# Kernel optimization log

Hardware: AMD Instinct MI355X
Metric: run time of the kernel (lower is better)

Reference implementation:

```python
import jax, jax.numpy as jnp
from jax import lax
import numpy as np

H = 16        # hidden_size == input_size
L = 8         # num_layers


def _lstm_layer(x_seq, Wih, Whh, bih, bhh):
    # x_seq: [B, T, H] -> outputs [B, T, H]; PyTorch gate order i,f,g,o
    B = x_seq.shape[0]
    b = bih + bhh  # [4H]

    def step(carry, xt):
        h, c = carry
        gates = xt @ Wih.T + h @ Whh.T + b  # [B, 4H]
        i, f, g, o = jnp.split(gates, 4, axis=-1)
        c = jax.nn.sigmoid(f) * c + jax.nn.sigmoid(i) * jnp.tanh(g)
        h = jax.nn.sigmoid(o) * jnp.tanh(c)
        return (h, c), h

    h0 = jnp.zeros((B, H), x_seq.dtype)
    (_, _), hs = lax.scan(step, (h0, h0), jnp.swapaxes(x_seq, 0, 1))
    return jnp.swapaxes(hs, 0, 1)  # [B, T, H]


def setup_inputs() -> dict:
    key = jax.random.key(0)
    ks = jax.random.split(key, 9)
    s = 1.0 / np.sqrt(H)  # PyTorch default init scale
    x = jax.random.normal(ks[0], (2048, 512, H), dtype=jnp.float32)
    W_ih = jax.random.uniform(ks[1], (L, 4 * H, H), jnp.float32, -s, s)
    W_hh = jax.random.uniform(ks[2], (L, 4 * H, H), jnp.float32, -s, s)
    b_ih = jax.random.uniform(ks[3], (L, 4 * H), jnp.float32, -s, s)
    b_hh = jax.random.uniform(ks[4], (L, 4 * H), jnp.float32, -s, s)
    Wp = jax.random.uniform(ks[5], (3, H), jnp.float32, -s, s)
    bp = jax.random.uniform(ks[6], (3,), jnp.float32, -s, s)
    Wo = jax.random.uniform(ks[7], (3, H), jnp.float32, -s, s)
    bo = jax.random.uniform(ks[8], (3,), jnp.float32, -s, s)
    return {"x": x, "W_ih": W_ih, "W_hh": W_hh, "b_ih": b_ih, "b_hh": b_hh,
            "Wp": Wp, "bp": bp, "Wo": Wo, "bo": bo}


def reference(x, W_ih, W_hh, b_ih, b_hh, Wp, bp, Wo, bo):
    h = x
    for l in range(L):  # fixed small layer count
        h = _lstm_layer(h, W_ih[l], W_hh[l], b_ih[l], b_hh[l])
    last = h[:, -1, :]                       # [B, H]
    position = last @ Wp.T + bp              # [B, 3]
    orientation = jnp.tanh(last @ Wo.T + bo) # [B, 3]
    return jnp.concatenate((position, orientation), axis=1)  # [B, 6]
```

## Files before the change

### kernel.cpp

```cpp
#include <hip/hip_runtime.h>
#include <math.h>

typedef _Float16 f16x8 __attribute__((ext_vector_type(8)));
typedef float    f32x4 __attribute__((ext_vector_type(4)));

constexpr int kT     = 512;
constexpr int kH     = 16;
constexpr int kL     = 8;
constexpr int kNB    = 4;
constexpr int kSlots = 8;
constexpr int kLyr   = kL + 1;
constexpr int kRows  = 5;
constexpr int kRowE  = 16;
constexpr int kSE    = kLyr * kRows * kRowE;
constexpr int kEpochs= 136;

constexpr float kL2E = 1.4426950408889634f;

__device__ __forceinline__ float ex2(float w)  { return __builtin_amdgcn_exp2f(w); }
__device__ __forceinline__ float rcpf(float e) { return __builtin_amdgcn_rcpf(e); }

__global__ __launch_bounds__(512, 4)
void lstm_e4(const float* __restrict__ x,
             const float* __restrict__ Wih, const float* __restrict__ Whh,
             const float* __restrict__ bih, const float* __restrict__ bhh,
             const float* __restrict__ Wp,  const float* __restrict__ bpos,
             const float* __restrict__ Wo,  const float* __restrict__ bori,
             float* __restrict__ out)
{
    const int tid  = threadIdx.x;
    const int l    = tid >> 6;
    const int lane = tid & 63;
    const int n    = lane & 15;
    const int q    = lane >> 4;
    const int bl   = n & 3;
    const int g2   = (n >> 2) & 1;
    const int hi   = n >> 3;
    const bool bact = ((q >> 1) == g2);

    __shared__ __align__(16) _Float16 hb[kSlots][kLyr][kRows][kRowE];

    {
        int* hz = (int*)&hb[0][0][0][0];
        for (int i = tid; i < (int)(sizeof(hb) / 4); i += 512) hz[i] = 0;
    }
    __syncthreads();

    const float asc = ((n & 3) == 2) ? (-2.0f * kL2E) : (-kL2E);
    auto loadA = [&](const float* W, int T) -> f16x8 {
        const int wrow = (n & 3) * 16 + (n >> 2) + 4 * (q >> 1) + 8 * T;
        const float* src = W + (size_t)l * 64 * kH + wrow * kH;
        f16x8 a;
        #pragma unroll
        for (int j = 0; j < 8; ++j)
            a[j] = (_Float16)(asc * src[(q & 1) * 8 + j]);
        return a;
    };
    const f16x8 A1T0 = loadA(Wih, 0), A1T1 = loadA(Wih, 1);
    const f16x8 A2T0 = loadA(Whh, 0), A2T1 = loadA(Whh, 1);

    const int u0b = q + 4 * g2;
    f32x4 biasT0, biasT1;
    #pragma unroll
    for (int r = 0; r < 4; ++r) {
        const float sc = (r == 2) ? (-2.0f * kL2E) : (-kL2E);
        const int g0 = l * 64 + r * 16 + u0b;
        biasT0[r] = sc * (bih[g0] + bhh[g0]);
        biasT1[r] = sc * (bih[g0 + 8] + bhh[g0 + 8]);
    }

    const int boff = (bact ? bl * kRowE : 4 * kRowE) + (q & 1) * 8;
    const _Float16* b1b = &hb[0][l    ][0][0] + boff;
    const _Float16* b2b = &hb[0][l + 1][0][0] + boff;
    const int um = u0b + 8 * hi;
    _Float16* hw = &hb[0][l + 1][bl][um];
    _Float16* xw = &hb[0][0][bl][um];

    const float* xg = x + ((size_t)(blockIdx.x * kNB + bl) * kT) * kH + um;
    float xr[4] = {0.f, 0.f, 0.f, 0.f};
    if (l == 0) {
        #pragma unroll
        for (int t = 0; t < 8; ++t)
            hb[t][0][bl][um] = (_Float16)xg[(size_t)t * kH];
        #pragma unroll
        for (int j = 0; j < 4; ++j)
            xr[j] = xg[(size_t)(8 + j) * kH];
    }

    f16x8 B2r;
    #pragma unroll
    for (int j = 0; j < 8; ++j) B2r[j] = (_Float16)0.f;
    float c0 = 0.f;
    int te   = -4 * l;
    int sOfs = (l & 1) ? 4 * kSE : 0;

    #pragma unroll 1
    for (int ep = 0; ep < kEpochs; ++ep) {
        const _Float16* b1p = b1b + sOfs;
        const _Float16* b2p = b2b + sOfs;
        _Float16* hwp = hw + sOfs;
        _Float16* xwp = xw + sOfs;

        #pragma unroll
        for (int j = 0; j < 4; ++j) {
            const int t = te + j;
            const bool active = ((unsigned)t < (unsigned)kT);

            const f16x8 B1 = *(const f16x8*)(b1p + j * kSE);

            f32x4 dInT0 = __builtin_amdgcn_mfma_f32_16x16x32_f16(A1T0, B1, biasT0, 0, 0, 0);
            f32x4 dInT1 = __builtin_amdgcn_mfma_f32_16x16x32_f16(A1T1, B1, biasT1, 0, 0, 0);
            f32x4 dT0   = __builtin_amdgcn_mfma_f32_16x16x32_f16(A2T0, B2r, dInT0, 0, 0, 0);
            f32x4 dT1   = __builtin_amdgcn_mfma_f32_16x16x32_f16(A2T1, B2r, dInT1, 0, 0, 0);

            f32x4 d;
            #pragma unroll
            for (int r = 0; r < 4; ++r) d[r] = hi ? dT1[r] : dT0[r];

            const float Ei = ex2(fminf(d[0], 40.0f));
            const float Ef = ex2(fminf(d[1], 40.0f));
            const float Eg = ex2(fminf(d[2], 40.0f));
            const float Eo = ex2(fminf(d[3], 60.0f));
            const float Dg = 1.0f + Eg;
            const float Df = 1.0f + Ef;
            const float P1  = fmaf(Ei, Dg, Dg);
            const float den = Df * P1;
            const float t2  = fmaf(-Eg, Df, Df);
            const float num = fmaf(c0, P1, t2);
            float cn = num * rcpf(den);
            cn = active ? cn : 0.0f;
            c0 = cn;
            const float ac = fminf(cn * (-2.0f * kL2E), 60.0f);
            const float Ec = ex2(ac);
            const float Do = 1.0f + Eo;
            const float R2 = rcpf(fmaf(Do, Ec, Do));
            const float h0 = fmaf(-Ec, R2, R2);

            *(hwp + j * kSE) = (_Float16)h0;
            B2r = *(const f16x8*)(b2p + j * kSE);

            if (l == 0) {
                *(xwp + j * kSE) = (_Float16)xr[j];
                int ti = te + 12 + j; if (ti > kT - 1) ti = kT - 1;
                xr[j] = xg[(size_t)ti * kH];
            }
        }

        te += 4;
        sOfs ^= 4 * kSE;
        asm volatile("s_waitcnt lgkmcnt(0)\n\ts_barrier" ::: "memory");
    }

    __syncthreads();

    if (l == kL - 1 && lane < 32) {
        const int bb = lane >> 3;
        const int r  = lane & 7;
        if (r < 6) {
            const bool  isP   = (r < 3);
            const float* wrow = isP ? (Wp + r * kH) : (Wo + (r - 3) * kH);
            float acc = isP ? bpos[r] : bori[r - 3];
            #pragma unroll
            for (int u = 0; u < kH; ++u)
                acc = fmaf((float)hb[7][kL][bb][u], wrow[u], acc);
            if (!isP) {
                const float Et = ex2(-2.0f * kL2E * acc);
                acc = fmaf(2.0f, rcpf(1.0f + Et), -1.0f);
            }
            out[(size_t)(blockIdx.x * kNB + bb) * 6 + r] = acc;
        }
    }
}

extern "C" void kernel_launch(void* const* d_in, const int* in_sizes, int n_in,
                              void* d_out, int out_size, void* d_ws, size_t ws_size,
                              hipStream_t stream) {
    const float* x    = (const float*)d_in[0];
    const float* Wih  = (const float*)d_in[1];
    const float* Whh  = (const float*)d_in[2];
    const float* bih  = (const float*)d_in[3];
    const float* bhh  = (const float*)d_in[4];
    const float* Wp   = (const float*)d_in[5];
    const float* bpos = (const float*)d_in[6];
    const float* Wo   = (const float*)d_in[7];
    const float* bori = (const float*)d_in[8];
    float* out = (float*)d_out;

    const int B = in_sizes[0] / (kT * kH);
    lstm_e4<<<dim3(B / kNB), dim3(512), 0, stream>>>(x, Wih, Whh, bih, bhh,
                                                     Wp, bpos, Wo, bori, out);
}
```

Measured before the change: 303.5 us.

## Pass recurrent hidden state via ds_bpermute and shrink layer wavefront to 2-step epochs

Each wave now builds its own recurrent h operand in registers, using a lane shuffle plus ds_bpermute, instead of reading it back from shared memory. The epoch drops from 4 timesteps to 2 and the layer skew halves from 4 to 2 steps per layer, so the pipeline fill and drain are shorter, at the cost of twice as many barriers. The barrier waits with lgkmcnt(4) so the outstanding bpermutes can overlap it. The aim is to take the LDS store-then-reload latency off the serial dependency chain between timesteps.

```diff
diff --git a/kernel.cpp b/kernel.cpp
--- a/kernel.cpp
+++ b/kernel.cpp
@@ -13,7 +13,7 @@
 constexpr int kRows  = 5;
 constexpr int kRowE  = 16;
 constexpr int kSE    = kLyr * kRows * kRowE;
-constexpr int kEpochs= 136;
+constexpr int kEp    = 263;
 
 constexpr float kL2E = 1.4426950408889634f;
 
@@ -21,12 +21,12 @@
 __device__ __forceinline__ float rcpf(float e) { return __builtin_amdgcn_rcpf(e); }
 
 __global__ __launch_bounds__(512, 4)
-void lstm_e4(const float* __restrict__ x,
-             const float* __restrict__ Wih, const float* __restrict__ Whh,
-             const float* __restrict__ bih, const float* __restrict__ bhh,
-             const float* __restrict__ Wp,  const float* __restrict__ bpos,
-             const float* __restrict__ Wo,  const float* __restrict__ bori,
-             float* __restrict__ out)
+void lstm_bp2(const float* __restrict__ x,
+              const float* __restrict__ Wih, const float* __restrict__ Whh,
+              const float* __restrict__ bih, const float* __restrict__ bhh,
+              const float* __restrict__ Wp,  const float* __restrict__ bpos,
+              const float* __restrict__ Wo,  const float* __restrict__ bori,
+              float* __restrict__ out)
 {
     const int tid  = threadIdx.x;
     const int l    = tid >> 6;
@@ -70,53 +70,62 @@
     }
 
     const int boff = (bact ? bl * kRowE : 4 * kRowE) + (q & 1) * 8;
-    const _Float16* b1b = &hb[0][l    ][0][0] + boff;
-    const _Float16* b2b = &hb[0][l + 1][0][0] + boff;
+    const _Float16* b1b = &hb[0][l][0][0] + boff;
     const int um = u0b + 8 * hi;
     _Float16* hw = &hb[0][l + 1][bl][um];
     _Float16* xw = &hb[0][0][bl][um];
 
+    int bpa[4];
+    #pragma unroll
+    for (int d = 0; d < 4; ++d) {
+        const int v0 = (q & 1) * 8 + 2 * d;
+        const int Lh = 16 * (v0 & 3) + bl + 4 * ((v0 >> 2) & 1) + 8 * (v0 >> 3);
+        bpa[d] = 4 * Lh;
+    }
+    const int msk = bact ? ~0 : 0;
+
     const float* xg = x + ((size_t)(blockIdx.x * kNB + bl) * kT) * kH + um;
-    float xr[4] = {0.f, 0.f, 0.f, 0.f};
+    float xr0 = 0.f, xr1 = 0.f, xr2 = 0.f, xr3 = 0.f;
     if (l == 0) {
         #pragma unroll
         for (int t = 0; t < 8; ++t)
             hb[t][0][bl][um] = (_Float16)xg[(size_t)t * kH];
-        #pragma unroll
-        for (int j = 0; j < 4; ++j)
-            xr[j] = xg[(size_t)(8 + j) * kH];
-    }
-
-    f16x8 B2r;
-    #pragma unroll
-    for (int j = 0; j < 8; ++j) B2r[j] = (_Float16)0.f;
+        xr0 = xg[ 8 * (size_t)kH];
+        xr1 = xg[ 9 * (size_t)kH];
+        xr2 = xg[10 * (size_t)kH];
+        xr3 = xg[11 * (size_t)kH];
+    }
+    __syncthreads();
+
+    int nb0 = 0, nb1 = 0, nb2 = 0, nb3 = 0;
     float c0 = 0.f;
-    int te   = -4 * l;
-    int sOfs = (l & 1) ? 4 * kSE : 0;
+    int te   = -2 * l;
+    int offA = ((-2 * l) & 7) * kSE;
 
     #pragma unroll 1
-    for (int ep = 0; ep < kEpochs; ++ep) {
-        const _Float16* b1p = b1b + sOfs;
-        const _Float16* b2p = b2b + sOfs;
-        _Float16* hwp = hw + sOfs;
-        _Float16* xwp = xw + sOfs;
-
-        #pragma unroll
-        for (int j = 0; j < 4; ++j) {
-            const int t = te + j;
-            const bool active = ((unsigned)t < (unsigned)kT);
-
-            const f16x8 B1 = *(const f16x8*)(b1p + j * kSE);
-
-            f32x4 dInT0 = __builtin_amdgcn_mfma_f32_16x16x32_f16(A1T0, B1, biasT0, 0, 0, 0);
-            f32x4 dInT1 = __builtin_amdgcn_mfma_f32_16x16x32_f16(A1T1, B1, biasT1, 0, 0, 0);
-            f32x4 dT0   = __builtin_amdgcn_mfma_f32_16x16x32_f16(A2T0, B2r, dInT0, 0, 0, 0);
-            f32x4 dT1   = __builtin_amdgcn_mfma_f32_16x16x32_f16(A2T1, B2r, dInT1, 0, 0, 0);
-
-            f32x4 d;
-            #pragma unroll
-            for (int r = 0; r < 4; ++r) d[r] = hi ? dT1[r] : dT0[r];
-
+    for (int ep = 0; ep < kEp; ++ep) {
+        const int offB = offA + kSE;
+        const bool activeA = ((unsigned)te       < (unsigned)kT);
+        const bool activeB = ((unsigned)(te + 1) < (unsigned)kT);
+
+        const f16x8 B1a = *(const f16x8*)(b1b + offA);
+        const f16x8 B1b = *(const f16x8*)(b1b + offB);
+
+        union { int i[4]; f16x8 v; } uA;
+        uA.i[0] = nb0 & msk; uA.i[1] = nb1 & msk;
+        uA.i[2] = nb2 & msk; uA.i[3] = nb3 & msk;
+        const f16x8 B2A = uA.v;
+
+        f32x4 dIn0 = __builtin_amdgcn_mfma_f32_16x16x32_f16(A1T0, B1a, biasT0, 0, 0, 0);
+        f32x4 dIn1 = __builtin_amdgcn_mfma_f32_16x16x32_f16(A1T1, B1a, biasT1, 0, 0, 0);
+        f32x4 dT0  = __builtin_amdgcn_mfma_f32_16x16x32_f16(A2T0, B2A, dIn0, 0, 0, 0);
+        f32x4 dT1  = __builtin_amdgcn_mfma_f32_16x16x32_f16(A2T1, B2A, dIn1, 0, 0, 0);
+        f32x4 d;
+        #pragma unroll
+        for (int r = 0; r < 4; ++r) d[r] = hi ? dT1[r] : dT0[r];
+
+        float hA;
+        {
             const float Ei = ex2(fminf(d[0], 40.0f));
             const float Ef = ex2(fminf(d[1], 40.0f));
             const float Eg = ex2(fminf(d[2], 40.0f));
@@ -128,27 +137,82 @@
             const float t2  = fmaf(-Eg, Df, Df);
             const float num = fmaf(c0, P1, t2);
             float cn = num * rcpf(den);
-            cn = active ? cn : 0.0f;
+            cn = activeA ? cn : 0.0f;
             c0 = cn;
             const float ac = fminf(cn * (-2.0f * kL2E), 60.0f);
             const float Ec = ex2(ac);
             const float Do = 1.0f + Eo;
             const float R2 = rcpf(fmaf(Do, Ec, Do));
-            const float h0 = fmaf(-Ec, R2, R2);
-
-            *(hwp + j * kSE) = (_Float16)h0;
-            B2r = *(const f16x8*)(b2p + j * kSE);
-
-            if (l == 0) {
-                *(xwp + j * kSE) = (_Float16)xr[j];
-                int ti = te + 12 + j; if (ti > kT - 1) ti = kT - 1;
-                xr[j] = xg[(size_t)ti * kH];
-            }
-        }
-
-        te += 4;
-        sOfs ^= 4 * kSE;
-        asm volatile("s_waitcnt lgkmcnt(0)\n\ts_barrier" ::: "memory");
+            hA = fmaf(-Ec, R2, R2);
+        }
+
+        *(hw + offA) = (_Float16)hA;
+        if (l == 0) *(xw + offA) = (_Float16)xr0;
+
+        const unsigned oA = (unsigned)__builtin_bit_cast(unsigned short, (_Float16)hA);
+        const unsigned pA = (unsigned)__shfl_xor((int)oA, 16, 64);
+        const unsigned packedA = (q & 1) ? ((oA << 16) | pA) : ((pA << 16) | oA);
+        union { int i[4]; f16x8 v; } uB;
+        uB.i[0] = __builtin_amdgcn_ds_bpermute(bpa[0], (int)packedA) & msk;
+        uB.i[1] = __builtin_amdgcn_ds_bpermute(bpa[1], (int)packedA) & msk;
+        uB.i[2] = __builtin_amdgcn_ds_bpermute(bpa[2], (int)packedA) & msk;
+        uB.i[3] = __builtin_amdgcn_ds_bpermute(bpa[3], (int)packedA) & msk;
+        const f16x8 B2B = uB.v;
+
+        dIn0 = __builtin_amdgcn_mfma_f32_16x16x32_f16(A1T0, B1b, biasT0, 0, 0, 0);
+        dIn1 = __builtin_amdgcn_mfma_f32_16x16x32_f16(A1T1, B1b, biasT1, 0, 0, 0);
+        dT0  = __builtin_amdgcn_mfma_f32_16x16x32_f16(A2T0, B2B, dIn0, 0, 0, 0);
+        dT1  = __builtin_amdgcn_mfma_f32_16x16x32_f16(A2T1, B2B, dIn1, 0, 0, 0);
+        #pragma unroll
+        for (int r = 0; r < 4; ++r) d[r] = hi ? dT1[r] : dT0[r];
+
+        float hB;
+        {
+            const float Ei = ex2(fminf(d[0], 40.0f));
+            const float Ef = ex2(fminf(d[1], 40.0f));
+            const float Eg = ex2(fminf(d[2], 40.0f));
+            const float Eo = ex2(fminf(d[3], 60.0f));
+            const float Dg = 1.0f + Eg;
+            const float Df = 1.0f + Ef;
+            const float P1  = fmaf(Ei, Dg, Dg);
+            const float den = Df * P1;
+            const float t2  = fmaf(-Eg, Df, Df);
+            const float num = fmaf(c0, P1, t2);
+            float cn = num * rcpf(den);
+            cn = activeB ? cn : 0.0f;
+            c0 = cn;
+            const float ac = fminf(cn * (-2.0f * kL2E), 60.0f);
+            const float Ec = ex2(ac);
+            const float Do = 1.0f + Eo;
+            const float R2 = rcpf(fmaf(Do, Ec, Do));
+            hB = fmaf(-Ec, R2, R2);
+        }
+
+        *(hw + offB) = (_Float16)hB;
+        if (l == 0) {
+            *(xw + offB) = (_Float16)xr1;
+            xr0 = xr2; xr1 = xr3;
+            int t2i = te + 12; if (t2i > kT - 1) t2i = kT - 1;
+            int t3i = te + 13; if (t3i > kT - 1) t3i = kT - 1;
+            xr2 = xg[(size_t)t2i * kH];
+            xr3 = xg[(size_t)t3i * kH];
+        }
+
+        __builtin_amdgcn_sched_barrier(0);
+
+        const unsigned oB = (unsigned)__builtin_bit_cast(unsigned short, (_Float16)hB);
+        const unsigned pB = (unsigned)__shfl_xor((int)oB, 16, 64);
+        const unsigned packedB = (q & 1) ? ((oB << 16) | pB) : ((pB << 16) | oB);
+        nb0 = __builtin_amdgcn_ds_bpermute(bpa[0], (int)packedB);
+        nb1 = __builtin_amdgcn_ds_bpermute(bpa[1], (int)packedB);
+        nb2 = __builtin_amdgcn_ds_bpermute(bpa[2], (int)packedB);
+        nb3 = __builtin_amdgcn_ds_bpermute(bpa[3], (int)packedB);
+        __builtin_amdgcn_sched_barrier(0);
+
+        te += 2;
+        offA += 2 * kSE; if (offA >= 8 * kSE) offA -= 8 * kSE;
+
+        asm volatile("s_waitcnt lgkmcnt(4)\n\ts_barrier" ::: "memory");
     }
 
     __syncthreads();
@@ -187,6 +251,6 @@
     float* out = (float*)d_out;
 
     const int B = in_sizes[0] / (kT * kH);
-    lstm_e4<<<dim3(B / kNB), dim3(512), 0, stream>>>(x, Wih, Whh, bih, bhh,
-                                                     Wp, bpos, Wo, bori, out);
+    lstm_bp2<<<dim3(B / kNB), dim3(512), 0, stream>>>(x, Wih, Whh, bih, bhh,
+                                                      Wp, bpos, Wo, bori, out);
 }
```

After: 369.8 us. 21.8% more time.
